# Kernel tuning notes

Measured on AMD Instinct MI355X. Metric: run time of the kernel, lower is better.

## Reference

```python
import jax, jax.numpy as jnp
import numpy as np

B, T, H, DK, DV = 4, 2048, 1024, 1024, 1024


def setup_inputs() -> dict:
    key = jax.random.key(0)
    ks = jax.random.split(key, 9)
    s = lambda fan_in: 1.0 / np.sqrt(fan_in)
    return {
        "y_all": jax.random.normal(ks[0], (B, T, H), dtype=jnp.float32),
        "Wq": jax.random.uniform(ks[1], (H, DK), jnp.float32, -s(H), s(H)),
        "bq": jax.random.uniform(ks[2], (DK,), jnp.float32, -s(H), s(H)),
        "Wk": jax.random.uniform(ks[3], (H, DK), jnp.float32, -s(H), s(H)),
        "bk": jax.random.uniform(ks[4], (DK,), jnp.float32, -s(H), s(H)),
        "Wv": jax.random.uniform(ks[5], (H, DV), jnp.float32, -s(H), s(H)),
        "bv": jax.random.uniform(ks[6], (DV,), jnp.float32, -s(H), s(H)),
        "Wo": jax.random.uniform(ks[7], (DV, H), jnp.float32, -s(DV), s(DV)),
        "bo": jax.random.uniform(ks[8], (H,), jnp.float32, -s(DV), s(DV)),
    }


def reference(y_all, Wq, bq, Wk, bk, Wv, bv, Wo, bo):
    # Fused causal attention equivalent to the per-timestep Python loop.
    dk = Wq.shape[1]
    q = (y_all @ Wq + bq) / jnp.sqrt(jnp.asarray(dk, y_all.dtype))  # [B,T,DK]
    k = y_all @ Wk + bk                                             # [B,T,DK]
    v = y_all @ Wv + bv                                             # [B,T,DV]
    scores = jnp.einsum("bqd,bkd->bqk", q, k)                       # [B,T,T]
    t = y_all.shape[1]
    causal = jnp.tril(jnp.ones((t, t), dtype=bool))                 # [T,T]
    scores = jnp.where(causal[None], scores, jnp.asarray(-jnp.inf, scores.dtype))
    w = jax.nn.softmax(scores, axis=-1)                             # [B,T,T]
    ctx = jnp.einsum("bqk,bkd->bqd", w, v)                          # [B,T,DV]
    return ctx @ Wo + bo                                            # [B,T,H]
```

## Files before the change

kernel.cpp:

```cpp
#include <hip/hip_runtime.h>
#include <hip/hip_bf16.h>
#include <cstdint>

#define DEVI __device__ __forceinline__

typedef __attribute__((ext_vector_type(8))) short bf16x8;
typedef __attribute__((ext_vector_type(4))) short bf16x4;
typedef __attribute__((ext_vector_type(4))) float f32x4;

DEVI short f2bf(float f) {
  unsigned u = __float_as_uint(f);
  u += 0x7fff + ((u >> 16) & 1);
  return (short)(u >> 16);
}
DEVI float bf2f(short s) { return __uint_as_float(((unsigned)(unsigned short)s) << 16); }

DEVI void gl_lds16(const short* g, short* l) {
  __builtin_amdgcn_global_load_lds((const __attribute__((address_space(1))) unsigned*)g,
                                   (__attribute__((address_space(3))) unsigned*)l, 16, 0, 0);
}

constexpr int BM = 128, BN = 128, BK = 64;

template<int MODE, int BIASMODE, bool OUTF32, int DECODE>
__global__ __launch_bounds__(256, 2)
void gemm_bt(const short* __restrict__ A, const short* __restrict__ B,
             void* __restrict__ Cv, const float* __restrict__ b0,
             float scale, int K, int lda, int ldb, int ldc,
             long long sA, long long sB, long long sC, int tdim)
{
  const int nwg = gridDim.x, orig = blockIdx.x;
  const int q8 = nwg >> 3, r8 = nwg & 7;
  const int xcd = orig & 7, idx8 = orig >> 3;
  const int wg = (xcd < r8 ? xcd * (q8 + 1) : r8 * (q8 + 1) + (xcd - r8) * q8) + idx8;
  const int bz = blockIdx.z;

  int bi = wg / tdim;
  const int bj = wg - bi * tdim;

  A += (long long)bz * sA;
  B += (long long)bz * sB;

  __shared__ __align__(16) short lA[2][BM * BK];
  __shared__ __align__(16) short lB[2][BN * BK];

  const int tid = threadIdx.x, wave = tid >> 6, lane = tid & 63;
  const int wr = wave >> 1, wc = wave & 1;
  const int brow = bi * BM, bcol = bj * BN;
  const int fr = lane & 15, h = lane >> 4;

  const int ck0 = ((h ^ (fr & 7))) * 8;
  const int swc = ((tid & 7) ^ ((tid >> 3) & 7)) * 8;
  const short* pA = A + (long long)(brow + (tid >> 3)) * lda + swc;
  const short* pB = B + (long long)(bcol + (tid >> 3)) * ldb + swc;

  f32x4 acc[4][4] = {};
  const int nt = K / BK;

  auto stage = [&](int buf, int t) {
    const long long ko = (long long)t * BK;
#pragma unroll
    for (int j = 0; j < 4; ++j)
      gl_lds16(pA + (long long)(j * 32) * lda + ko, &lA[buf][j * 2048 + tid * 8]);
#pragma unroll
    for (int j = 0; j < 4; ++j)
      gl_lds16(pB + (long long)(j * 32) * ldb + ko, &lB[buf][j * 2048 + tid * 8]);
  };

  stage(0, 0);
  __syncthreads();

  int cur = 0;
  for (int t = 0; t < nt; ++t) {
    if (t + 1 < nt) stage(cur ^ 1, t + 1);

    const short* bufA = lA[cur];
    const short* bufB = lB[cur];
    bf16x8 af[4], bg[4];
#pragma unroll
    for (int m = 0; m < 4; ++m)
      af[m] = *(const bf16x8*)&bufA[(wr * 64 + m * 16 + fr) * BK + ck0];
#pragma unroll
    for (int n = 0; n < 4; ++n)
      bg[n] = *(const bf16x8*)&bufB[(wc * 64 + n * 16 + fr) * BK + ck0];
#pragma unroll
    for (int m = 0; m < 4; ++m)
#pragma unroll
      for (int n = 0; n < 4; ++n)
        acc[m][n] = __builtin_amdgcn_mfma_f32_16x16x32_bf16(af[m], bg[n], acc[m][n], 0, 0, 0);
#pragma unroll
    for (int m = 0; m < 4; ++m)
      af[m] = *(const bf16x8*)&bufA[((wr * 64 + m * 16 + fr) * BK + ck0) ^ 32];
#pragma unroll
    for (int n = 0; n < 4; ++n)
      bg[n] = *(const bf16x8*)&bufB[((wc * 64 + n * 16 + fr) * BK + ck0) ^ 32];
#pragma unroll
    for (int m = 0; m < 4; ++m)
#pragma unroll
      for (int n = 0; n < 4; ++n)
        acc[m][n] = __builtin_amdgcn_mfma_f32_16x16x32_bf16(af[m], bg[n], acc[m][n], 0, 0, 0);

    __syncthreads();
    cur ^= 1;
  }

  const int lrow = h * 4;
  float* Cf = (float*)Cv + (long long)bz * sC;
  short* Cs = (short*)Cv + (long long)bz * sC;
  int colg[4]; float bvv[4];
#pragma unroll
  for (int n = 0; n < 4; ++n) {
    colg[n] = bcol + wc * 64 + n * 16 + fr;
    bvv[n] = (BIASMODE == 1) ? b0[colg[n]] : 0.f;
  }
#pragma unroll
  for (int m = 0; m < 4; ++m) {
    const int row = brow + wr * 64 + m * 16 + lrow;
#pragma unroll
    for (int j = 0; j < 4; ++j) {
#pragma unroll
      for (int n = 0; n < 4; ++n) {
        const float val = (acc[m][n][j] + bvv[n]) * scale;
        if constexpr (OUTF32) Cf[(long long)(row + j) * ldc + colg[n]] = val;
        else                  Cs[(long long)(row + j) * ldc + colg[n]] = f2bf(val);
      }
    }
  }
}

__global__ __launch_bounds__(256, 4)
void gemm_g(const short* __restrict__ ybf, const short* __restrict__ MTb,
            short* __restrict__ G, const float* __restrict__ wvec)
{
  const int orig = blockIdx.x;
  const int xcd = orig & 7, idx8 = orig >> 3;
  const int wg = xcd * 64 + idx8;
  const int bi = wg >> 3, bj = wg & 7;

  __shared__ __align__(16) short lA[BM * BK];
  __shared__ __align__(16) short lB[BN * BK];

  const int tid = threadIdx.x, wave = tid >> 6, lane = tid & 63;
  const int wr = wave >> 1, wc = wave & 1;
  const int brow = bi * BM, bcol = bj * BN;
  const int fr = lane & 15, h = lane >> 4;

  const int ck0 = ((h ^ (fr & 7))) * 8;
  const int swc = ((tid & 7) ^ ((tid >> 3) & 7)) * 8;
  const short* pA = ybf + (long long)(brow + (tid >> 3)) * 1024 + swc;
  const short* pB = MTb + (long long)(bcol + (tid >> 3)) * 1024 + swc;

  f32x4 acc[4][4] = {};

  for (int t = 0; t < 16; ++t) {
    const long long ko = (long long)t * BK;
#pragma unroll
    for (int j = 0; j < 4; ++j)
      gl_lds16(pA + (long long)(j * 32) * 1024 + ko, &lA[j * 2048 + tid * 8]);
#pragma unroll
    for (int j = 0; j < 4; ++j)
      gl_lds16(pB + (long long)(j * 32) * 1024 + ko, &lB[j * 2048 + tid * 8]);
    __syncthreads();

    bf16x8 af[4], bg[4];
#pragma unroll
    for (int m = 0; m < 4; ++m)
      af[m] = *(const bf16x8*)&lA[(wr * 64 + m * 16 + fr) * BK + ck0];
#pragma unroll
    for (int n = 0; n < 4; ++n)
      bg[n] = *(const bf16x8*)&lB[(wc * 64 + n * 16 + fr) * BK + ck0];
#pragma unroll
    for (int m = 0; m < 4; ++m)
#pragma unroll
      for (int n = 0; n < 4; ++n)
        acc[m][n] = __builtin_amdgcn_mfma_f32_16x16x32_bf16(af[m], bg[n], acc[m][n], 0, 0, 0);
#pragma unroll
    for (int m = 0; m < 4; ++m)
      af[m] = *(const bf16x8*)&lA[((wr * 64 + m * 16 + fr) * BK + ck0) ^ 32];
#pragma unroll
    for (int n = 0; n < 4; ++n)
      bg[n] = *(const bf16x8*)&lB[((wc * 64 + n * 16 + fr) * BK + ck0) ^ 32];
#pragma unroll
    for (int m = 0; m < 4; ++m)
#pragma unroll
      for (int n = 0; n < 4; ++n)
        acc[m][n] = __builtin_amdgcn_mfma_f32_16x16x32_bf16(af[m], bg[n], acc[m][n], 0, 0, 0);
    __syncthreads();
  }

  const int lrow = h * 4;
  int colg[4]; float bvv[4];
#pragma unroll
  for (int n = 0; n < 4; ++n) {
    colg[n] = bcol + wc * 64 + n * 16 + fr;
    bvv[n] = wvec[colg[n]];
  }
#pragma unroll
  for (int m = 0; m < 4; ++m) {
    const int row = brow + wr * 64 + m * 16 + lrow;
#pragma unroll
    for (int j = 0; j < 4; ++j)
#pragma unroll
      for (int n = 0; n < 4; ++n)
        G[(long long)(row + j) * 1024 + colg[n]] =
            f2bf((acc[m][n][j] + bvv[n]) * (1.f / 32.f));
  }
}

__global__ __launch_bounds__(256, 4)
void gemm_sz(const short* __restrict__ G, const short* __restrict__ ybf,
             const short* __restrict__ WvoT, short* __restrict__ scores,
             short* __restrict__ zT)
{
  const int orig = blockIdx.x;
  const int xcd = orig & 7, idx8 = orig >> 3;
  const int wg = xcd * 132 + idx8;

  const short *A, *B; short* C; int ldc, bi, bj;
  if (wg < 544) {
    const int z = wg / 136, t = wg - z * 136;
    int b = (int)((__fsqrt_rn(8.f * (float)t + 1.f) - 1.f) * 0.5f);
    if ((b + 1) * (b + 2) / 2 <= t) ++b;
    if (b * (b + 1) / 2 > t) --b;
    bi = b; bj = t - b * (b + 1) / 2;
    A = G + (long long)z * 2048 * 1024;
    B = ybf + (long long)z * 2048 * 1024;
    C = scores + (long long)z * 2048 * 2048;
    ldc = 2048;
  } else {
    const int lwg = wg - 544;
    bi = lwg >> 6; bj = lwg & 63;
    A = WvoT; B = ybf; C = zT; ldc = 8192;
  }

  __shared__ __align__(16) short lA[BM * BK];
  __shared__ __align__(16) short lB[BN * BK];

  const int tid = threadIdx.x, wave = tid >> 6, lane = tid & 63;
  const int wr = wave >> 1, wc = wave & 1;
  const int brow = bi * BM, bcol = bj * BN;
  const int fr = lane & 15, h = lane >> 4;

  const int ck0 = ((h ^ (fr & 7))) * 8;
  const int swc = ((tid & 7) ^ ((tid >> 3) & 7)) * 8;
  const short* pA = A + (long long)(brow + (tid >> 3)) * 1024 + swc;
  const short* pB = B + (long long)(bcol + (tid >> 3)) * 1024 + swc;

  f32x4 acc[4][4] = {};

  for (int t = 0; t < 16; ++t) {
    const long long ko = (long long)t * BK;
#pragma unroll
    for (int j = 0; j < 4; ++j)
      gl_lds16(pA + (long long)(j * 32) * 1024 + ko, &lA[j * 2048 + tid * 8]);
#pragma unroll
    for (int j = 0; j < 4; ++j)
      gl_lds16(pB + (long long)(j * 32) * 1024 + ko, &lB[j * 2048 + tid * 8]);
    __syncthreads();

    bf16x8 af[4], bg[4];
#pragma unroll
    for (int m = 0; m < 4; ++m)
      af[m] = *(const bf16x8*)&lA[(wr * 64 + m * 16 + fr) * BK + ck0];
#pragma unroll
    for (int n = 0; n < 4; ++n)
      bg[n] = *(const bf16x8*)&lB[(wc * 64 + n * 16 + fr) * BK + ck0];
#pragma unroll
    for (int m = 0; m < 4; ++m)
#pragma unroll
      for (int n = 0; n < 4; ++n)
        acc[m][n] = __builtin_amdgcn_mfma_f32_16x16x32_bf16(af[m], bg[n], acc[m][n], 0, 0, 0);
#pragma unroll
    for (int m = 0; m < 4; ++m)
      af[m] = *(const bf16x8*)&lA[((wr * 64 + m * 16 + fr) * BK + ck0) ^ 32];
#pragma unroll
    for (int n = 0; n < 4; ++n)
      bg[n] = *(const bf16x8*)&lB[((wc * 64 + n * 16 + fr) * BK + ck0) ^ 32];
#pragma unroll
    for (int m = 0; m < 4; ++m)
#pragma unroll
      for (int n = 0; n < 4; ++n)
        acc[m][n] = __builtin_amdgcn_mfma_f32_16x16x32_bf16(af[m], bg[n], acc[m][n], 0, 0, 0);
    __syncthreads();
  }

  const int lrow = h * 4;
  int colg[4];
#pragma unroll
  for (int n = 0; n < 4; ++n) colg[n] = bcol + wc * 64 + n * 16 + fr;
#pragma unroll
  for (int m = 0; m < 4; ++m) {
    const int row = brow + wr * 64 + m * 16 + lrow;
#pragma unroll
    for (int j = 0; j < 4; ++j)
#pragma unroll
      for (int n = 0; n < 4; ++n)
        C[(long long)(row + j) * ldc + colg[n]] = f2bf(acc[m][n][j]);
  }
}

__global__ __launch_bounds__(256, 6)
void gemm_pv(const short* __restrict__ scores, const short* __restrict__ zT,
             float* __restrict__ out, const float* __restrict__ bias)
{
  const int orig = blockIdx.x;
  const int xcd = orig & 7, idx8 = orig >> 3;
  const int z = xcd >> 1;
  const int bi = ((idx8 >> 4) << 1) | (xcd & 1);
  const int bj = idx8 & 15;

  const short* A = scores + (long long)z * 2048 * 2048;
  const int nt = bi + 1;

  __shared__ __align__(16) short lA[64 * 64];
  __shared__ __align__(16) short lB[64 * 64];

  const int tid = threadIdx.x, wave = tid >> 6, lane = tid & 63;
  const int wm = wave >> 1, wn = wave & 1;
  const int brow = bi * 64, bcol = bj * 64;
  const int fr = lane & 15, h = lane >> 4;

  const int ck0 = ((h ^ (fr & 7))) * 8;
  const int swc = ((tid & 7) ^ ((tid >> 3) & 7)) * 8;
  const short* pA = A + (long long)(brow + (tid >> 3)) * 2048 + swc;
  const short* pB = zT + (long long)(bcol + (tid >> 3)) * 8192 + z * 2048 + swc;

  f32x4 acc[2][2] = {};

  for (int t = 0; t < nt; ++t) {
    const long long ko = (long long)t * 64;
#pragma unroll
    for (int j = 0; j < 2; ++j)
      gl_lds16(pA + (long long)(j * 32) * 2048 + ko, &lA[j * 2048 + tid * 8]);
#pragma unroll
    for (int j = 0; j < 2; ++j)
      gl_lds16(pB + (long long)(j * 32) * 8192 + ko, &lB[j * 2048 + tid * 8]);
    __syncthreads();

    bf16x8 af[2], bg[2];
#pragma unroll
    for (int m = 0; m < 2; ++m)
      af[m] = *(const bf16x8*)&lA[(wm * 32 + m * 16 + fr) * 64 + ck0];
#pragma unroll
    for (int n = 0; n < 2; ++n)
      bg[n] = *(const bf16x8*)&lB[(wn * 32 + n * 16 + fr) * 64 + ck0];
#pragma unroll
    for (int m = 0; m < 2; ++m)
#pragma unroll
      for (int n = 0; n < 2; ++n)
        acc[m][n] = __builtin_amdgcn_mfma_f32_16x16x32_bf16(af[m], bg[n], acc[m][n], 0, 0, 0);
#pragma unroll
    for (int m = 0; m < 2; ++m)
      af[m] = *(const bf16x8*)&lA[((wm * 32 + m * 16 + fr) * 64 + ck0) ^ 32];
#pragma unroll
    for (int n = 0; n < 2; ++n)
      bg[n] = *(const bf16x8*)&lB[((wn * 32 + n * 16 + fr) * 64 + ck0) ^ 32];
#pragma unroll
    for (int m = 0; m < 2; ++m)
#pragma unroll
      for (int n = 0; n < 2; ++n)
        acc[m][n] = __builtin_amdgcn_mfma_f32_16x16x32_bf16(af[m], bg[n], acc[m][n], 0, 0, 0);
    __syncthreads();
  }

  const int lrow = h * 4;
  int colg[2]; float bvv[2];
#pragma unroll
  for (int n = 0; n < 2; ++n) {
    colg[n] = bcol + wn * 32 + n * 16 + fr;
    bvv[n] = bias[colg[n]];
  }
#pragma unroll
  for (int m = 0; m < 2; ++m) {
    const int row = brow + wm * 32 + m * 16 + lrow;
#pragma unroll
    for (int j = 0; j < 4; ++j)
#pragma unroll
      for (int n = 0; n < 2; ++n)
        out[(long long)(z * 2048 + row + j) * 1024 + colg[n]] = acc[m][n][j] + bvv[n];
  }
}

__global__ __launch_bounds__(256)
void softmax_causal_bf16_k(short* __restrict__ sc)
{
  const int T = 2048;
  const long long row = blockIdx.x;
  const int t = (int)(row & (T - 1));
  short* ps = sc + row * (long long)T;
  const int tid = threadIdx.x, wave = tid >> 6, lane = tid & 63;
  const int c0 = tid * 8;
  const int wlim = ((t >> 6) + 1) << 6;

  bf16x8 v = {};
  if (c0 <= t) v = *(const bf16x8*)&ps[c0];
  float x[8];
#pragma unroll
  for (int j = 0; j < 8; ++j) x[j] = bf2f(v[j]);

  float mx = -3.0e38f;
#pragma unroll
  for (int j = 0; j < 8; ++j) if (c0 + j <= t) mx = fmaxf(mx, x[j]);
#pragma unroll
  for (int o = 32; o; o >>= 1) mx = fmaxf(mx, __shfl_xor(mx, o, 64));
  __shared__ float red[8];
  if (lane == 0) red[wave] = mx;
  __syncthreads();
  const float M = fmaxf(fmaxf(red[0], red[1]), fmaxf(red[2], red[3]));

  float e[8], s = 0.f;
#pragma unroll
  for (int j = 0; j < 8; ++j) { e[j] = (c0 + j <= t) ? __expf(x[j] - M) : 0.f; s += e[j]; }
#pragma unroll
  for (int o = 32; o; o >>= 1) s += __shfl_xor(s, o, 64);
  if (lane == 0) red[4 + wave] = s;
  __syncthreads();
  const float inv = 1.f / (red[4] + red[5] + red[6] + red[7]);

  if (c0 < wlim) {
    bf16x8 ov;
#pragma unroll
    for (int j = 0; j < 8; ++j) ov[j] = f2bf(e[j] * inv);
    *(bf16x8*)&ps[c0] = ov;
  }
}

__global__ __launch_bounds__(256)
void cvt_y_k(const float* __restrict__ y, short* __restrict__ ybf)
{
  const long long i = (long long)blockIdx.x * 256 + threadIdx.x;
  const float4 v0 = ((const float4*)y)[i * 2];
  const float4 v1 = ((const float4*)y)[i * 2 + 1];
  bf16x8 o;
  o[0] = f2bf(v0.x); o[1] = f2bf(v0.y); o[2] = f2bf(v0.z); o[3] = f2bf(v0.w);
  o[4] = f2bf(v1.x); o[5] = f2bf(v1.y); o[6] = f2bf(v1.z); o[7] = f2bf(v1.w);
  ((bf16x8*)ybf)[i] = o;
}

__global__ __launch_bounds__(256)
void cvt_w_all_k(const float* __restrict__ w0, const float* __restrict__ w1,
                 const float* __restrict__ w2, const float* __restrict__ w3,
                 short* __restrict__ o0, short* __restrict__ o1,
                 short* __restrict__ o2, short* __restrict__ o3)
{
  const int tx = threadIdx.x & 31, ty = threadIdx.x >> 5;
  const int r0 = blockIdx.y * 32, c0 = blockIdx.x * 32;
  if (blockIdx.z != 2) {
    const float* in = (blockIdx.z == 0) ? w0 : (blockIdx.z == 1 ? w1 : w3);
    short* out      = (blockIdx.z == 0) ? o0 : (blockIdx.z == 1 ? o1 : o3);
#pragma unroll
    for (int i = 0; i < 4; ++i)
      out[(long long)(r0 + ty + 8 * i) * 1024 + c0 + tx] =
          f2bf(in[(long long)(r0 + ty + 8 * i) * 1024 + c0 + tx]);
    return;
  }
  __shared__ float tile[32][33];
#pragma unroll
  for (int i = 0; i < 4; ++i)
    tile[ty + 8 * i][tx] = w2[(long long)(r0 + ty + 8 * i) * 1024 + c0 + tx];
  __syncthreads();
#pragma unroll
  for (int i = 0; i < 4; ++i)
    o2[(long long)(c0 + ty + 8 * i) * 1024 + r0 + tx] = f2bf(tile[tx][ty + 8 * i]);
}

__global__ __launch_bounds__(256)
void bias_init_k(const float* __restrict__ bo, float* __restrict__ outb)
{
  const int j = blockIdx.x * 256 + threadIdx.x;
  outb[j] = bo[j];
}

__global__ __launch_bounds__(256)
void bias_fold_k(const float* __restrict__ bv, const float* __restrict__ Wo,
                 float* __restrict__ outb)
{
  const int r0 = blockIdx.x * 16;
  const int c4 = threadIdx.x;
  float4 acc = make_float4(0.f, 0.f, 0.f, 0.f);
  for (int r = 0; r < 16; ++r) {
    const float s = bv[r0 + r];
    const float4 w = ((const float4*)(Wo + (long long)(r0 + r) * 1024))[c4];
    acc.x += s * w.x; acc.y += s * w.y; acc.z += s * w.z; acc.w += s * w.w;
  }
  atomicAdd(&outb[c4 * 4 + 0], acc.x);
  atomicAdd(&outb[c4 * 4 + 1], acc.y);
  atomicAdd(&outb[c4 * 4 + 2], acc.z);
  atomicAdd(&outb[c4 * 4 + 3], acc.w);
}

__global__ __launch_bounds__(256)
void wkbq_gemv_k(const float* __restrict__ Wk, const float* __restrict__ bq,
                 float* __restrict__ w)
{
  const int row = blockIdx.x, tid = threadIdx.x;
  const float4 a = ((const float4*)(Wk + (long long)row * 1024))[tid];
  const float4 b = ((const float4*)bq)[tid];
  float s = a.x * b.x + a.y * b.y + a.z * b.z + a.w * b.w;
#pragma unroll
  for (int o = 32; o; o >>= 1) s += __shfl_xor(s, o, 64);
  __shared__ float red[4];
  if ((tid & 63) == 0) red[tid >> 6] = s;
  __syncthreads();
  if (tid == 0) w[row] = red[0] + red[1] + red[2] + red[3];
}

__global__ __launch_bounds__(256)
void combine4_k(const float* __restrict__ p, short* __restrict__ out)
{
  const long long i = (long long)blockIdx.x * 256 + threadIdx.x;
  const float4 a = ((const float4*)p)[i];
  const float4 b = ((const float4*)(p + 1048576))[i];
  const float4 c = ((const float4*)(p + 2097152))[i];
  const float4 d = ((const float4*)(p + 3145728))[i];
  bf16x4 o;
  o[0] = f2bf(a.x + b.x + c.x + d.x);
  o[1] = f2bf(a.y + b.y + c.y + d.y);
  o[2] = f2bf(a.z + b.z + c.z + d.z);
  o[3] = f2bf(a.w + b.w + c.w + d.w);
  ((bf16x4*)out)[i] = o;
}

extern "C" void kernel_launch(void* const* d_in, const int* in_sizes, int n_in,
                              void* d_out, int out_size, void* d_ws, size_t ws_size,
                              hipStream_t stream)
{
  (void)in_sizes; (void)n_in; (void)out_size; (void)ws_size;
  const float* y  = (const float*)d_in[0];
  const float* Wq = (const float*)d_in[1];
  const float* bq = (const float*)d_in[2];
  const float* Wk = (const float*)d_in[3];
  const float* bk = (const float*)d_in[4];
  const float* Wv = (const float*)d_in[5];
  const float* bv = (const float*)d_in[6];
  const float* Wo = (const float*)d_in[7];
  const float* bo = (const float*)d_in[8];
  float* out = (float*)d_out;
  (void)bk;

  const int T = 2048;
  const long long MT = 8192;
  const long long MM = 1048576;

  short* ws    = (short*)d_ws;
  short* ybf   = ws;
  short* WqBf  = ybf + MT * 1024;
  short* WkBf  = WqBf + MM;
  short* WoT   = WkBf + MM;
  short* WvBf  = WoT + MM;
  short* MTb   = WvBf + MM;
  short* WvoT  = MTb + MM;
  short* G     = WvoT + MM;
  short* zT    = G + MT * 1024;
  short* scores = zT + MT * 1024;
  float* bvWoBo = (float*)(scores + 4ll * T * T);
  float* wvec   = bvWoBo + 1024;
  float* part   = wvec + 1024;

  cvt_y_k<<<4096, 256, 0, stream>>>(y, ybf);
  cvt_w_all_k<<<dim3(32, 32, 4), 256, 0, stream>>>(
      Wq, Wk, Wo, Wv, WqBf, WkBf, WoT, WvBf);
  bias_init_k<<<4, 256, 0, stream>>>(bo, bvWoBo);
  bias_fold_k<<<64, 256, 0, stream>>>(bv, Wo, bvWoBo);
  wkbq_gemv_k<<<1024, 256, 0, stream>>>(Wk, bq, wvec);

  gemm_bt<0, 0, true, 0><<<dim3(64, 1, 4), 256, 0, stream>>>(
      WkBf, WqBf, part, nullptr, 1.f, 256, 1024, 1024, 1024,
      256, 256, 1048576, 8);
  combine4_k<<<1024, 256, 0, stream>>>(part, MTb);

  gemm_bt<0, 0, true, 0><<<dim3(64, 1, 4), 256, 0, stream>>>(
      WoT, WvBf, part, nullptr, 1.f, 256, 1024, 1024, 1024,
      256, 256, 1048576, 8);
  combine4_k<<<1024, 256, 0, stream>>>(part, WvoT);

  gemm_g<<<512, 256, 0, stream>>>(ybf, MTb, G, wvec);

  gemm_sz<<<1056, 256, 0, stream>>>(G, ybf, WvoT, scores, zT);

  softmax_causal_bf16_k<<<(int)MT, 256, 0, stream>>>(scores);

  gemm_pv<<<2048, 256, 0, stream>>>(scores, zT, out, bvWoBo);
}
```

Measured before the change: 175.3 us.

## Merge prep kernels and weight GEMMs, retile G and score GEMMs for more workgroups

Merges the five conversion and bias pre-pass kernels into one launch, and merges the two split-K weight-product GEMMs and their two combine passes into single launches. gemm_g and gemm_sz are replaced by new versions launched with twice as many workgroups, likely smaller tiles, and the bias add for bo is folded into the final PV epilogue. The goal is fewer kernel launches and better CU occupancy on the mid-sized GEMMs. The cost is more branching inside the merged kernels and possibly less data reuse per tile.

New measurement: 162.6 us. 1.08x faster.

```diff
diff --git a/kernel.cpp b/kernel.cpp
--- a/kernel.cpp
+++ b/kernel.cpp
@@ -20,225 +20,29 @@
                                    (__attribute__((address_space(3))) unsigned*)l, 16, 0, 0);
 }
 
-constexpr int BM = 128, BN = 128, BK = 64;
-
-template<int MODE, int BIASMODE, bool OUTF32, int DECODE>
-__global__ __launch_bounds__(256, 2)
-void gemm_bt(const short* __restrict__ A, const short* __restrict__ B,
-             void* __restrict__ Cv, const float* __restrict__ b0,
-             float scale, int K, int lda, int ldb, int ldc,
-             long long sA, long long sB, long long sC, int tdim)
-{
-  const int nwg = gridDim.x, orig = blockIdx.x;
-  const int q8 = nwg >> 3, r8 = nwg & 7;
-  const int xcd = orig & 7, idx8 = orig >> 3;
-  const int wg = (xcd < r8 ? xcd * (q8 + 1) : r8 * (q8 + 1) + (xcd - r8) * q8) + idx8;
-  const int bz = blockIdx.z;
-
-  int bi = wg / tdim;
-  const int bj = wg - bi * tdim;
-
-  A += (long long)bz * sA;
-  B += (long long)bz * sB;
-
-  __shared__ __align__(16) short lA[2][BM * BK];
-  __shared__ __align__(16) short lB[2][BN * BK];
-
-  const int tid = threadIdx.x, wave = tid >> 6, lane = tid & 63;
-  const int wr = wave >> 1, wc = wave & 1;
-  const int brow = bi * BM, bcol = bj * BN;
-  const int fr = lane & 15, h = lane >> 4;
-
-  const int ck0 = ((h ^ (fr & 7))) * 8;
-  const int swc = ((tid & 7) ^ ((tid >> 3) & 7)) * 8;
-  const short* pA = A + (long long)(brow + (tid >> 3)) * lda + swc;
-  const short* pB = B + (long long)(bcol + (tid >> 3)) * ldb + swc;
-
-  f32x4 acc[4][4] = {};
-  const int nt = K / BK;
-
-  auto stage = [&](int buf, int t) {
-    const long long ko = (long long)t * BK;
-#pragma unroll
-    for (int j = 0; j < 4; ++j)
-      gl_lds16(pA + (long long)(j * 32) * lda + ko, &lA[buf][j * 2048 + tid * 8]);
-#pragma unroll
-    for (int j = 0; j < 4; ++j)
-      gl_lds16(pB + (long long)(j * 32) * ldb + ko, &lB[buf][j * 2048 + tid * 8]);
-  };
-
-  stage(0, 0);
-  __syncthreads();
-
-  int cur = 0;
-  for (int t = 0; t < nt; ++t) {
-    if (t + 1 < nt) stage(cur ^ 1, t + 1);
-
-    const short* bufA = lA[cur];
-    const short* bufB = lB[cur];
-    bf16x8 af[4], bg[4];
-#pragma unroll
-    for (int m = 0; m < 4; ++m)
-      af[m] = *(const bf16x8*)&bufA[(wr * 64 + m * 16 + fr) * BK + ck0];
-#pragma unroll
-    for (int n = 0; n < 4; ++n)
-      bg[n] = *(const bf16x8*)&bufB[(wc * 64 + n * 16 + fr) * BK + ck0];
-#pragma unroll
-    for (int m = 0; m < 4; ++m)
-#pragma unroll
-      for (int n = 0; n < 4; ++n)
-        acc[m][n] = __builtin_amdgcn_mfma_f32_16x16x32_bf16(af[m], bg[n], acc[m][n], 0, 0, 0);
-#pragma unroll
-    for (int m = 0; m < 4; ++m)
-      af[m] = *(const bf16x8*)&bufA[((wr * 64 + m * 16 + fr) * BK + ck0) ^ 32];
-#pragma unroll
-    for (int n = 0; n < 4; ++n)
-      bg[n] = *(const bf16x8*)&bufB[((wc * 64 + n * 16 + fr) * BK + ck0) ^ 32];
-#pragma unroll
-    for (int m = 0; m < 4; ++m)
-#pragma unroll
-      for (int n = 0; n < 4; ++n)
-        acc[m][n] = __builtin_amdgcn_mfma_f32_16x16x32_bf16(af[m], bg[n], acc[m][n], 0, 0, 0);
-
-    __syncthreads();
-    cur ^= 1;
-  }
-
-  const int lrow = h * 4;
-  float* Cf = (float*)Cv + (long long)bz * sC;
-  short* Cs = (short*)Cv + (long long)bz * sC;
-  int colg[4]; float bvv[4];
-#pragma unroll
-  for (int n = 0; n < 4; ++n) {
-    colg[n] = bcol + wc * 64 + n * 16 + fr;
-    bvv[n] = (BIASMODE == 1) ? b0[colg[n]] : 0.f;
-  }
-#pragma unroll
-  for (int m = 0; m < 4; ++m) {
-    const int row = brow + wr * 64 + m * 16 + lrow;
-#pragma unroll
-    for (int j = 0; j < 4; ++j) {
-#pragma unroll
-      for (int n = 0; n < 4; ++n) {
-        const float val = (acc[m][n][j] + bvv[n]) * scale;
-        if constexpr (OUTF32) Cf[(long long)(row + j) * ldc + colg[n]] = val;
-        else                  Cs[(long long)(row + j) * ldc + colg[n]] = f2bf(val);
-      }
-    }
-  }
-}
 
 __global__ __launch_bounds__(256, 4)
-void gemm_g(const short* __restrict__ ybf, const short* __restrict__ MTb,
-            short* __restrict__ G, const float* __restrict__ wvec)
+void gemm_ww(const short* __restrict__ WkBf, const short* __restrict__ WqBf,
+             const short* __restrict__ WoT, const short* __restrict__ WvBf,
+             float* __restrict__ partM, float* __restrict__ partW)
 {
   const int orig = blockIdx.x;
   const int xcd = orig & 7, idx8 = orig >> 3;
   const int wg = xcd * 64 + idx8;
-  const int bi = wg >> 3, bj = wg & 7;
-
-  __shared__ __align__(16) short lA[BM * BK];
-  __shared__ __align__(16) short lB[BN * BK];
+  const int job = wg >> 8, rem = wg & 255;
+  const int z = rem >> 6, t = rem & 63;
+  const int bi = t >> 3, bj = t & 7;
+
+  const short* A = job ? WoT  : WkBf;
+  const short* B = job ? WvBf : WqBf;
+  float* Cf = (job ? partW : partM) + (long long)z * 1048576;
+
+  __shared__ __align__(16) short lA[128 * 64];
+  __shared__ __align__(16) short lB[128 * 64];
 
   const int tid = threadIdx.x, wave = tid >> 6, lane = tid & 63;
   const int wr = wave >> 1, wc = wave & 1;
-  const int brow = bi * BM, bcol = bj * BN;
-  const int fr = lane & 15, h = lane >> 4;
-
-  const int ck0 = ((h ^ (fr & 7))) * 8;
-  const int swc = ((tid & 7) ^ ((tid >> 3) & 7)) * 8;
-  const short* pA = ybf + (long long)(brow + (tid >> 3)) * 1024 + swc;
-  const short* pB = MTb + (long long)(bcol + (tid >> 3)) * 1024 + swc;
-
-  f32x4 acc[4][4] = {};
-
-  for (int t = 0; t < 16; ++t) {
-    const long long ko = (long long)t * BK;
-#pragma unroll
-    for (int j = 0; j < 4; ++j)
-      gl_lds16(pA + (long long)(j * 32) * 1024 + ko, &lA[j * 2048 + tid * 8]);
-#pragma unroll
-    for (int j = 0; j < 4; ++j)
-      gl_lds16(pB + (long long)(j * 32) * 1024 + ko, &lB[j * 2048 + tid * 8]);
-    __syncthreads();
-
-    bf16x8 af[4], bg[4];
-#pragma unroll
-    for (int m = 0; m < 4; ++m)
-      af[m] = *(const bf16x8*)&lA[(wr * 64 + m * 16 + fr) * BK + ck0];
-#pragma unroll
-    for (int n = 0; n < 4; ++n)
-      bg[n] = *(const bf16x8*)&lB[(wc * 64 + n * 16 + fr) * BK + ck0];
-#pragma unroll
-    for (int m = 0; m < 4; ++m)
-#pragma unroll
-      for (int n = 0; n < 4; ++n)
-        acc[m][n] = __builtin_amdgcn_mfma_f32_16x16x32_bf16(af[m], bg[n], acc[m][n], 0, 0, 0);
-#pragma unroll
-    for (int m = 0; m < 4; ++m)
-      af[m] = *(const bf16x8*)&lA[((wr * 64 + m * 16 + fr) * BK + ck0) ^ 32];
-#pragma unroll
-    for (int n = 0; n < 4; ++n)
-      bg[n] = *(const bf16x8*)&lB[((wc * 64 + n * 16 + fr) * BK + ck0) ^ 32];
-#pragma unroll
-    for (int m = 0; m < 4; ++m)
-#pragma unroll
-      for (int n = 0; n < 4; ++n)
-        acc[m][n] = __builtin_amdgcn_mfma_f32_16x16x32_bf16(af[m], bg[n], acc[m][n], 0, 0, 0);
-    __syncthreads();
-  }
-
-  const int lrow = h * 4;
-  int colg[4]; float bvv[4];
-#pragma unroll
-  for (int n = 0; n < 4; ++n) {
-    colg[n] = bcol + wc * 64 + n * 16 + fr;
-    bvv[n] = wvec[colg[n]];
-  }
-#pragma unroll
-  for (int m = 0; m < 4; ++m) {
-    const int row = brow + wr * 64 + m * 16 + lrow;
-#pragma unroll
-    for (int j = 0; j < 4; ++j)
-#pragma unroll
-      for (int n = 0; n < 4; ++n)
-        G[(long long)(row + j) * 1024 + colg[n]] =
-            f2bf((acc[m][n][j] + bvv[n]) * (1.f / 32.f));
-  }
-}
-
-__global__ __launch_bounds__(256, 4)
-void gemm_sz(const short* __restrict__ G, const short* __restrict__ ybf,
-             const short* __restrict__ WvoT, short* __restrict__ scores,
-             short* __restrict__ zT)
-{
-  const int orig = blockIdx.x;
-  const int xcd = orig & 7, idx8 = orig >> 3;
-  const int wg = xcd * 132 + idx8;
-
-  const short *A, *B; short* C; int ldc, bi, bj;
-  if (wg < 544) {
-    const int z = wg / 136, t = wg - z * 136;
-    int b = (int)((__fsqrt_rn(8.f * (float)t + 1.f) - 1.f) * 0.5f);
-    if ((b + 1) * (b + 2) / 2 <= t) ++b;
-    if (b * (b + 1) / 2 > t) --b;
-    bi = b; bj = t - b * (b + 1) / 2;
-    A = G + (long long)z * 2048 * 1024;
-    B = ybf + (long long)z * 2048 * 1024;
-    C = scores + (long long)z * 2048 * 2048;
-    ldc = 2048;
-  } else {
-    const int lwg = wg - 544;
-    bi = lwg >> 6; bj = lwg & 63;
-    A = WvoT; B = ybf; C = zT; ldc = 8192;
-  }
-
-  __shared__ __align__(16) short lA[BM * BK];
-  __shared__ __align__(16) short lB[BN * BK];
-
-  const int tid = threadIdx.x, wave = tid >> 6, lane = tid & 63;
-  const int wr = wave >> 1, wc = wave & 1;
-  const int brow = bi * BM, bcol = bj * BN;
+  const int brow = bi * 128, bcol = bj * 128;
   const int fr = lane & 15, h = lane >> 4;
 
   const int ck0 = ((h ^ (fr & 7))) * 8;
@@ -247,9 +51,10 @@
   const short* pB = B + (long long)(bcol + (tid >> 3)) * 1024 + swc;
 
   f32x4 acc[4][4] = {};
-
-  for (int t = 0; t < 16; ++t) {
-    const long long ko = (long long)t * BK;
+  const long long ko0 = (long long)z * 256;
+
+  for (int t2 = 0; t2 < 4; ++t2) {
+    const long long ko = ko0 + t2 * 64;
 #pragma unroll
     for (int j = 0; j < 4; ++j)
       gl_lds16(pA + (long long)(j * 32) * 1024 + ko, &lA[j * 2048 + tid * 8]);
@@ -261,10 +66,10 @@
     bf16x8 af[4], bg[4];
 #pragma unroll
     for (int m = 0; m < 4; ++m)
-      af[m] = *(const bf16x8*)&lA[(wr * 64 + m * 16 + fr) * BK + ck0];
+      af[m] = *(const bf16x8*)&lA[(wr * 64 + m * 16 + fr) * 64 + ck0];
 #pragma unroll
     for (int n = 0; n < 4; ++n)
-      bg[n] = *(const bf16x8*)&lB[(wc * 64 + n * 16 + fr) * BK + ck0];
+      bg[n] = *(const bf16x8*)&lB[(wc * 64 + n * 16 + fr) * 64 + ck0];
 #pragma unroll
     for (int m = 0; m < 4; ++m)
 #pragma unroll
@@ -272,10 +77,10 @@
         acc[m][n] = __builtin_amdgcn_mfma_f32_16x16x32_bf16(af[m], bg[n], acc[m][n], 0, 0, 0);
 #pragma unroll
     for (int m = 0; m < 4; ++m)
-      af[m] = *(const bf16x8*)&lA[((wr * 64 + m * 16 + fr) * BK + ck0) ^ 32];
+      af[m] = *(const bf16x8*)&lA[((wr * 64 + m * 16 + fr) * 64 + ck0) ^ 32];
 #pragma unroll
     for (int n = 0; n < 4; ++n)
-      bg[n] = *(const bf16x8*)&lB[((wc * 64 + n * 16 + fr) * BK + ck0) ^ 32];
+      bg[n] = *(const bf16x8*)&lB[((wc * 64 + n * 16 + fr) * 64 + ck0) ^ 32];
 #pragma unroll
     for (int m = 0; m < 4; ++m)
 #pragma unroll
@@ -285,9 +90,6 @@
   }
 
   const int lrow = h * 4;
-  int colg[4];
-#pragma unroll
-  for (int n = 0; n < 4; ++n) colg[n] = bcol + wc * 64 + n * 16 + fr;
 #pragma unroll
   for (int m = 0; m < 4; ++m) {
     const int row = brow + wr * 64 + m * 16 + lrow;
@@ -295,220 +97,18 @@
     for (int j = 0; j < 4; ++j)
 #pragma unroll
       for (int n = 0; n < 4; ++n)
-        C[(long long)(row + j) * ldc + colg[n]] = f2bf(acc[m][n][j]);
-  }
-}
-
-__global__ __launch_bounds__(256, 6)
-void gemm_pv(const short* __restrict__ scores, const short* __restrict__ zT,
-             float* __restrict__ out, const float* __restrict__ bias)
-{
-  const int orig = blockIdx.x;
-  const int xcd = orig & 7, idx8 = orig >> 3;
-  const int z = xcd >> 1;
-  const int bi = ((idx8 >> 4) << 1) | (xcd & 1);
-  const int bj = idx8 & 15;
-
-  const short* A = scores + (long long)z * 2048 * 2048;
-  const int nt = bi + 1;
-
-  __shared__ __align__(16) short lA[64 * 64];
-  __shared__ __align__(16) short lB[64 * 64];
-
-  const int tid = threadIdx.x, wave = tid >> 6, lane = tid & 63;
-  const int wm = wave >> 1, wn = wave & 1;
-  const int brow = bi * 64, bcol = bj * 64;
-  const int fr = lane & 15, h = lane >> 4;
-
-  const int ck0 = ((h ^ (fr & 7))) * 8;
-  const int swc = ((tid & 7) ^ ((tid >> 3) & 7)) * 8;
-  const short* pA = A + (long long)(brow + (tid >> 3)) * 2048 + swc;
-  const short* pB = zT + (long long)(bcol + (tid >> 3)) * 8192 + z * 2048 + swc;
-
-  f32x4 acc[2][2] = {};
-
-  for (int t = 0; t < nt; ++t) {
-    const long long ko = (long long)t * 64;
-#pragma unroll
-    for (int j = 0; j < 2; ++j)
-      gl_lds16(pA + (long long)(j * 32) * 2048 + ko, &lA[j * 2048 + tid * 8]);
-#pragma unroll
-    for (int j = 0; j < 2; ++j)
-      gl_lds16(pB + (long long)(j * 32) * 8192 + ko, &lB[j * 2048 + tid * 8]);
-    __syncthreads();
-
-    bf16x8 af[2], bg[2];
-#pragma unroll
-    for (int m = 0; m < 2; ++m)
-      af[m] = *(const bf16x8*)&lA[(wm * 32 + m * 16 + fr) * 64 + ck0];
-#pragma unroll
-    for (int n = 0; n < 2; ++n)
-      bg[n] = *(const bf16x8*)&lB[(wn * 32 + n * 16 + fr) * 64 + ck0];
-#pragma unroll
-    for (int m = 0; m < 2; ++m)
-#pragma unroll
-      for (int n = 0; n < 2; ++n)
-        acc[m][n] = __builtin_amdgcn_mfma_f32_16x16x32_bf16(af[m], bg[n], acc[m][n], 0, 0, 0);
-#pragma unroll
-    for (int m = 0; m < 2; ++m)
-      af[m] = *(const bf16x8*)&lA[((wm * 32 + m * 16 + fr) * 64 + ck0) ^ 32];
-#pragma unroll
-    for (int n = 0; n < 2; ++n)
-      bg[n] = *(const bf16x8*)&lB[((wn * 32 + n * 16 + fr) * 64 + ck0) ^ 32];
-#pragma unroll
-    for (int m = 0; m < 2; ++m)
-#pragma unroll
-      for (int n = 0; n < 2; ++n)
-        acc[m][n] = __builtin_amdgcn_mfma_f32_16x16x32_bf16(af[m], bg[n], acc[m][n], 0, 0, 0);
-    __syncthreads();
-  }
-
-  const int lrow = h * 4;
-  int colg[2]; float bvv[2];
-#pragma unroll
-  for (int n = 0; n < 2; ++n) {
-    colg[n] = bcol + wn * 32 + n * 16 + fr;
-    bvv[n] = bias[colg[n]];
-  }
-#pragma unroll
-  for (int m = 0; m < 2; ++m) {
-    const int row = brow + wm * 32 + m * 16 + lrow;
-#pragma unroll
-    for (int j = 0; j < 4; ++j)
-#pragma unroll
-      for (int n = 0; n < 2; ++n)
-        out[(long long)(z * 2048 + row + j) * 1024 + colg[n]] = acc[m][n][j] + bvv[n];
+        Cf[(long long)(row + j) * 1024 + bcol + wc * 64 + n * 16 + fr] = acc[m][n][j];
   }
 }
 
 __global__ __launch_bounds__(256)
-void softmax_causal_bf16_k(short* __restrict__ sc)
-{
-  const int T = 2048;
-  const long long row = blockIdx.x;
-  const int t = (int)(row & (T - 1));
-  short* ps = sc + row * (long long)T;
-  const int tid = threadIdx.x, wave = tid >> 6, lane = tid & 63;
-  const int c0 = tid * 8;
-  const int wlim = ((t >> 6) + 1) << 6;
-
-  bf16x8 v = {};
-  if (c0 <= t) v = *(const bf16x8*)&ps[c0];
-  float x[8];
-#pragma unroll
-  for (int j = 0; j < 8; ++j) x[j] = bf2f(v[j]);
-
-  float mx = -3.0e38f;
-#pragma unroll
-  for (int j = 0; j < 8; ++j) if (c0 + j <= t) mx = fmaxf(mx, x[j]);
-#pragma unroll
-  for (int o = 32; o; o >>= 1) mx = fmaxf(mx, __shfl_xor(mx, o, 64));
-  __shared__ float red[8];
-  if (lane == 0) red[wave] = mx;
-  __syncthreads();
-  const float M = fmaxf(fmaxf(red[0], red[1]), fmaxf(red[2], red[3]));
-
-  float e[8], s = 0.f;
-#pragma unroll
-  for (int j = 0; j < 8; ++j) { e[j] = (c0 + j <= t) ? __expf(x[j] - M) : 0.f; s += e[j]; }
-#pragma unroll
-  for (int o = 32; o; o >>= 1) s += __shfl_xor(s, o, 64);
-  if (lane == 0) red[4 + wave] = s;
-  __syncthreads();
-  const float inv = 1.f / (red[4] + red[5] + red[6] + red[7]);
-
-  if (c0 < wlim) {
-    bf16x8 ov;
-#pragma unroll
-    for (int j = 0; j < 8; ++j) ov[j] = f2bf(e[j] * inv);
-    *(bf16x8*)&ps[c0] = ov;
-  }
-}
-
-__global__ __launch_bounds__(256)
-void cvt_y_k(const float* __restrict__ y, short* __restrict__ ybf)
-{
-  const long long i = (long long)blockIdx.x * 256 + threadIdx.x;
-  const float4 v0 = ((const float4*)y)[i * 2];
-  const float4 v1 = ((const float4*)y)[i * 2 + 1];
-  bf16x8 o;
-  o[0] = f2bf(v0.x); o[1] = f2bf(v0.y); o[2] = f2bf(v0.z); o[3] = f2bf(v0.w);
-  o[4] = f2bf(v1.x); o[5] = f2bf(v1.y); o[6] = f2bf(v1.z); o[7] = f2bf(v1.w);
-  ((bf16x8*)ybf)[i] = o;
-}
-
-__global__ __launch_bounds__(256)
-void cvt_w_all_k(const float* __restrict__ w0, const float* __restrict__ w1,
-                 const float* __restrict__ w2, const float* __restrict__ w3,
-                 short* __restrict__ o0, short* __restrict__ o1,
-                 short* __restrict__ o2, short* __restrict__ o3)
-{
-  const int tx = threadIdx.x & 31, ty = threadIdx.x >> 5;
-  const int r0 = blockIdx.y * 32, c0 = blockIdx.x * 32;
-  if (blockIdx.z != 2) {
-    const float* in = (blockIdx.z == 0) ? w0 : (blockIdx.z == 1 ? w1 : w3);
-    short* out      = (blockIdx.z == 0) ? o0 : (blockIdx.z == 1 ? o1 : o3);
-#pragma unroll
-    for (int i = 0; i < 4; ++i)
-      out[(long long)(r0 + ty + 8 * i) * 1024 + c0 + tx] =
-          f2bf(in[(long long)(r0 + ty + 8 * i) * 1024 + c0 + tx]);
-    return;
-  }
-  __shared__ float tile[32][33];
-#pragma unroll
-  for (int i = 0; i < 4; ++i)
-    tile[ty + 8 * i][tx] = w2[(long long)(r0 + ty + 8 * i) * 1024 + c0 + tx];
-  __syncthreads();
-#pragma unroll
-  for (int i = 0; i < 4; ++i)
-    o2[(long long)(c0 + ty + 8 * i) * 1024 + r0 + tx] = f2bf(tile[tx][ty + 8 * i]);
-}
-
-__global__ __launch_bounds__(256)
-void bias_init_k(const float* __restrict__ bo, float* __restrict__ outb)
-{
-  const int j = blockIdx.x * 256 + threadIdx.x;
-  outb[j] = bo[j];
-}
-
-__global__ __launch_bounds__(256)
-void bias_fold_k(const float* __restrict__ bv, const float* __restrict__ Wo,
-                 float* __restrict__ outb)
-{
-  const int r0 = blockIdx.x * 16;
-  const int c4 = threadIdx.x;
-  float4 acc = make_float4(0.f, 0.f, 0.f, 0.f);
-  for (int r = 0; r < 16; ++r) {
-    const float s = bv[r0 + r];
-    const float4 w = ((const float4*)(Wo + (long long)(r0 + r) * 1024))[c4];
-    acc.x += s * w.x; acc.y += s * w.y; acc.z += s * w.z; acc.w += s * w.w;
-  }
-  atomicAdd(&outb[c4 * 4 + 0], acc.x);
-  atomicAdd(&outb[c4 * 4 + 1], acc.y);
-  atomicAdd(&outb[c4 * 4 + 2], acc.z);
-  atomicAdd(&outb[c4 * 4 + 3], acc.w);
-}
-
-__global__ __launch_bounds__(256)
-void wkbq_gemv_k(const float* __restrict__ Wk, const float* __restrict__ bq,
-                 float* __restrict__ w)
-{
-  const int row = blockIdx.x, tid = threadIdx.x;
-  const float4 a = ((const float4*)(Wk + (long long)row * 1024))[tid];
-  const float4 b = ((const float4*)bq)[tid];
-  float s = a.x * b.x + a.y * b.y + a.z * b.z + a.w * b.w;
-#pragma unroll
-  for (int o = 32; o; o >>= 1) s += __shfl_xor(s, o, 64);
-  __shared__ float red[4];
-  if ((tid & 63) == 0) red[tid >> 6] = s;
-  __syncthreads();
-  if (tid == 0) w[row] = red[0] + red[1] + red[2] + red[3];
-}
-
-__global__ __launch_bounds__(256)
-void combine4_k(const float* __restrict__ p, short* __restrict__ out)
-{
-  const long long i = (long long)blockIdx.x * 256 + threadIdx.x;
+void combine_ww(const float* __restrict__ partM, const float* __restrict__ partW,
+                short* __restrict__ MTb, short* __restrict__ WvoT)
+{
+  const int wg = blockIdx.x;
+  const float* p = (wg < 1024) ? partM : partW;
+  short* out = (wg < 1024) ? MTb : WvoT;
+  const long long i = (long long)(wg & 1023) * 256 + threadIdx.x;
   const float4 a = ((const float4*)p)[i];
   const float4 b = ((const float4*)(p + 1048576))[i];
   const float4 c = ((const float4*)(p + 2097152))[i];
@@ -519,6 +119,373 @@
   o[2] = f2bf(a.z + b.z + c.z + d.z);
   o[3] = f2bf(a.w + b.w + c.w + d.w);
   ((bf16x4*)out)[i] = o;
+}
+
+__global__ __launch_bounds__(256, 6)
+void gemm_g2(const short* __restrict__ ybf, const short* __restrict__ MTb,
+             short* __restrict__ G, const float* __restrict__ wvec)
+{
+  const int orig = blockIdx.x;
+  const int xcd = orig & 7, idx8 = orig >> 3;
+  const int wg = xcd * 128 + idx8;
+  const int bi = wg >> 4, bj = wg & 15;
+
+  __shared__ __align__(16) short lA[128 * 64];
+  __shared__ __align__(16) short lB[64 * 64];
+
+  const int tid = threadIdx.x, wave = tid >> 6, lane = tid & 63;
+  const int wr = wave >> 1, wc = wave & 1;
+  const int brow = bi * 128, bcol = bj * 64;
+  const int fr = lane & 15, h = lane >> 4;
+
+  const int ck0 = ((h ^ (fr & 7))) * 8;
+  const int swc = ((tid & 7) ^ ((tid >> 3) & 7)) * 8;
+  const short* pA = ybf + (long long)(brow + (tid >> 3)) * 1024 + swc;
+  const short* pB = MTb + (long long)(bcol + (tid >> 3)) * 1024 + swc;
+
+  f32x4 acc[4][2] = {};
+
+  for (int t = 0; t < 16; ++t) {
+    const long long ko = (long long)t * 64;
+#pragma unroll
+    for (int j = 0; j < 4; ++j)
+      gl_lds16(pA + (long long)(j * 32) * 1024 + ko, &lA[j * 2048 + tid * 8]);
+#pragma unroll
+    for (int j = 0; j < 2; ++j)
+      gl_lds16(pB + (long long)(j * 32) * 1024 + ko, &lB[j * 2048 + tid * 8]);
+    __syncthreads();
+
+    bf16x8 af[4], bg[2];
+#pragma unroll
+    for (int m = 0; m < 4; ++m)
+      af[m] = *(const bf16x8*)&lA[(wr * 64 + m * 16 + fr) * 64 + ck0];
+#pragma unroll
+    for (int n = 0; n < 2; ++n)
+      bg[n] = *(const bf16x8*)&lB[(wc * 32 + n * 16 + fr) * 64 + ck0];
+#pragma unroll
+    for (int m = 0; m < 4; ++m)
+#pragma unroll
+      for (int n = 0; n < 2; ++n)
+        acc[m][n] = __builtin_amdgcn_mfma_f32_16x16x32_bf16(af[m], bg[n], acc[m][n], 0, 0, 0);
+#pragma unroll
+    for (int m = 0; m < 4; ++m)
+      af[m] = *(const bf16x8*)&lA[((wr * 64 + m * 16 + fr) * 64 + ck0) ^ 32];
+#pragma unroll
+    for (int n = 0; n < 2; ++n)
+      bg[n] = *(const bf16x8*)&lB[((wc * 32 + n * 16 + fr) * 64 + ck0) ^ 32];
+#pragma unroll
+    for (int m = 0; m < 4; ++m)
+#pragma unroll
+      for (int n = 0; n < 2; ++n)
+        acc[m][n] = __builtin_amdgcn_mfma_f32_16x16x32_bf16(af[m], bg[n], acc[m][n], 0, 0, 0);
+    __syncthreads();
+  }
+
+  const int lrow = h * 4;
+  int colg[2]; float bvv[2];
+#pragma unroll
+  for (int n = 0; n < 2; ++n) {
+    colg[n] = bcol + wc * 32 + n * 16 + fr;
+    bvv[n] = wvec[colg[n]];
+  }
+#pragma unroll
+  for (int m = 0; m < 4; ++m) {
+    const int row = brow + wr * 64 + m * 16 + lrow;
+#pragma unroll
+    for (int j = 0; j < 4; ++j)
+#pragma unroll
+      for (int n = 0; n < 2; ++n)
+        G[(long long)(row + j) * 1024 + colg[n]] =
+            f2bf((acc[m][n][j] + bvv[n]) * (1.f / 32.f));
+  }
+}
+
+__global__ __launch_bounds__(256, 6)
+void gemm_sz2(const short* __restrict__ G, const short* __restrict__ ybf,
+              const short* __restrict__ WvoT, short* __restrict__ scores,
+              short* __restrict__ zT)
+{
+  const int orig = blockIdx.x;
+  const int xcd = orig & 7, idx8 = orig >> 3;
+  const int wg = xcd * 264 + idx8;
+
+  const short *A, *B; short* C; int ldc, bi, bj;
+  if (wg < 1088) {
+    const int z = wg / 272, t = wg - z * 272;
+    int b = (int)((__fsqrt_rn(4.f * (float)t + 1.f) - 1.f) * 0.5f);
+    if ((b + 1) * (b + 2) <= t) ++b;
+    if (b * (b + 1) > t) --b;
+    bi = b; bj = t - b * (b + 1);
+    A = G + (long long)z * 2048 * 1024;
+    B = ybf + (long long)z * 2048 * 1024;
+    C = scores + (long long)z * 2048 * 2048;
+    ldc = 2048;
+  } else {
+    const int lwg = wg - 1088;
+    bi = lwg >> 7; bj = lwg & 127;
+    A = WvoT; B = ybf; C = zT; ldc = 8192;
+  }
+
+  __shared__ __align__(16) short lA[128 * 64];
+  __shared__ __align__(16) short lB[64 * 64];
+
+  const int tid = threadIdx.x, wave = tid >> 6, lane = tid & 63;
+  const int wr = wave >> 1, wc = wave & 1;
+  const int brow = bi * 128, bcol = bj * 64;
+  const int fr = lane & 15, h = lane >> 4;
+
+  const int ck0 = ((h ^ (fr & 7))) * 8;
+  const int swc = ((tid & 7) ^ ((tid >> 3) & 7)) * 8;
+  const short* pA = A + (long long)(brow + (tid >> 3)) * 1024 + swc;
+  const short* pB = B + (long long)(bcol + (tid >> 3)) * 1024 + swc;
+
+  f32x4 acc[4][2] = {};
+
+  for (int t = 0; t < 16; ++t) {
+    const long long ko = (long long)t * 64;
+#pragma unroll
+    for (int j = 0; j < 4; ++j)
+      gl_lds16(pA + (long long)(j * 32) * 1024 + ko, &lA[j * 2048 + tid * 8]);
+#pragma unroll
+    for (int j = 0; j < 2; ++j)
+      gl_lds16(pB + (long long)(j * 32) * 1024 + ko, &lB[j * 2048 + tid * 8]);
+    __syncthreads();
+
+    bf16x8 af[4], bg[2];
+#pragma unroll
+    for (int m = 0; m < 4; ++m)
+      af[m] = *(const bf16x8*)&lA[(wr * 64 + m * 16 + fr) * 64 + ck0];
+#pragma unroll
+    for (int n = 0; n < 2; ++n)
+      bg[n] = *(const bf16x8*)&lB[(wc * 32 + n * 16 + fr) * 64 + ck0];
+#pragma unroll
+    for (int m = 0; m < 4; ++m)
+#pragma unroll
+      for (int n = 0; n < 2; ++n)
+        acc[m][n] = __builtin_amdgcn_mfma_f32_16x16x32_bf16(af[m], bg[n], acc[m][n], 0, 0, 0);
+#pragma unroll
+    for (int m = 0; m < 4; ++m)
+      af[m] = *(const bf16x8*)&lA[((wr * 64 + m * 16 + fr) * 64 + ck0) ^ 32];
+#pragma unroll
+    for (int n = 0; n < 2; ++n)
+      bg[n] = *(const bf16x8*)&lB[((wc * 32 + n * 16 + fr) * 64 + ck0) ^ 32];
+#pragma unroll
+    for (int m = 0; m < 4; ++m)
+#pragma unroll
+      for (int n = 0; n < 2; ++n)
+        acc[m][n] = __builtin_amdgcn_mfma_f32_16x16x32_bf16(af[m], bg[n], acc[m][n], 0, 0, 0);
+    __syncthreads();
+  }
+
+  const int lrow = h * 4;
+  int colg[2];
+#pragma unroll
+  for (int n = 0; n < 2; ++n) colg[n] = bcol + wc * 32 + n * 16 + fr;
+#pragma unroll
+  for (int m = 0; m < 4; ++m) {
+    const int row = brow + wr * 64 + m * 16 + lrow;
+#pragma unroll
+    for (int j = 0; j < 4; ++j)
+#pragma unroll
+      for (int n = 0; n < 2; ++n)
+        C[(long long)(row + j) * ldc + colg[n]] = f2bf(acc[m][n][j]);
+  }
+}
+
+__global__ __launch_bounds__(256, 6)
+void gemm_pv(const short* __restrict__ scores, const short* __restrict__ zT,
+             float* __restrict__ out, const float* __restrict__ bo,
+             const float* __restrict__ bvWo)
+{
+  const int orig = blockIdx.x;
+  const int xcd = orig & 7, idx8 = orig >> 3;
+  const int z = xcd >> 1;
+  const int bi = ((idx8 >> 4) << 1) | (xcd & 1);
+  const int bj = idx8 & 15;
+
+  const short* A = scores + (long long)z * 2048 * 2048;
+  const int nt = bi + 1;
+
+  __shared__ __align__(16) short lA[64 * 64];
+  __shared__ __align__(16) short lB[64 * 64];
+
+  const int tid = threadIdx.x, wave = tid >> 6, lane = tid & 63;
+  const int wm = wave >> 1, wn = wave & 1;
+  const int brow = bi * 64, bcol = bj * 64;
+  const int fr = lane & 15, h = lane >> 4;
+
+  const int ck0 = ((h ^ (fr & 7))) * 8;
+  const int swc = ((tid & 7) ^ ((tid >> 3) & 7)) * 8;
+  const short* pA = A + (long long)(brow + (tid >> 3)) * 2048 + swc;
+  const short* pB = zT + (long long)(bcol + (tid >> 3)) * 8192 + z * 2048 + swc;
+
+  f32x4 acc[2][2] = {};
+
+  for (int t = 0; t < nt; ++t) {
+    const long long ko = (long long)t * 64;
+#pragma unroll
+    for (int j = 0; j < 2; ++j)
+      gl_lds16(pA + (long long)(j * 32) * 2048 + ko, &lA[j * 2048 + tid * 8]);
+#pragma unroll
+    for (int j = 0; j < 2; ++j)
+      gl_lds16(pB + (long long)(j * 32) * 8192 + ko, &lB[j * 2048 + tid * 8]);
+    __syncthreads();
+
+    bf16x8 af[2], bg[2];
+#pragma unroll
+    for (int m = 0; m < 2; ++m)
+      af[m] = *(const bf16x8*)&lA[(wm * 32 + m * 16 + fr) * 64 + ck0];
+#pragma unroll
+    for (int n = 0; n < 2; ++n)
+      bg[n] = *(const bf16x8*)&lB[(wn * 32 + n * 16 + fr) * 64 + ck0];
+#pragma unroll
+    for (int m = 0; m < 2; ++m)
+#pragma unroll
+      for (int n = 0; n < 2; ++n)
+        acc[m][n] = __builtin_amdgcn_mfma_f32_16x16x32_bf16(af[m], bg[n], acc[m][n], 0, 0, 0);
+#pragma unroll
+    for (int m = 0; m < 2; ++m)
+      af[m] = *(const bf16x8*)&lA[((wm * 32 + m * 16 + fr) * 64 + ck0) ^ 32];
+#pragma unroll
+    for (int n = 0; n < 2; ++n)
+      bg[n] = *(const bf16x8*)&lB[((wn * 32 + n * 16 + fr) * 64 + ck0) ^ 32];
+#pragma unroll
+    for (int m = 0; m < 2; ++m)
+#pragma unroll
+      for (int n = 0; n < 2; ++n)
+        acc[m][n] = __builtin_amdgcn_mfma_f32_16x16x32_bf16(af[m], bg[n], acc[m][n], 0, 0, 0);
+    __syncthreads();
+  }
+
+  const int lrow = h * 4;
+  int colg[2]; float bvv[2];
+#pragma unroll
+  for (int n = 0; n < 2; ++n) {
+    colg[n] = bcol + wn * 32 + n * 16 + fr;
+    bvv[n] = bo[colg[n]] + bvWo[colg[n]];
+  }
+#pragma unroll
+  for (int m = 0; m < 2; ++m) {
+    const int row = brow + wm * 32 + m * 16 + lrow;
+#pragma unroll
+    for (int j = 0; j < 4; ++j)
+#pragma unroll
+      for (int n = 0; n < 2; ++n)
+        out[(long long)(z * 2048 + row + j) * 1024 + colg[n]] = acc[m][n][j] + bvv[n];
+  }
+}
+
+__global__ __launch_bounds__(256)
+void softmax_causal_bf16_k(short* __restrict__ sc)
+{
+  const int T = 2048;
+  const long long row = blockIdx.x;
+  const int t = (int)(row & (T - 1));
+  short* ps = sc + row * (long long)T;
+  const int tid = threadIdx.x, wave = tid >> 6, lane = tid & 63;
+  const int c0 = tid * 8;
+  const int wlim = ((t >> 6) + 1) << 6;
+
+  bf16x8 v = {};
+  if (c0 <= t) v = *(const bf16x8*)&ps[c0];
+  float x[8];
+#pragma unroll
+  for (int j = 0; j < 8; ++j) x[j] = bf2f(v[j]);
+
+  float mx = -3.0e38f;
+#pragma unroll
+  for (int j = 0; j < 8; ++j) if (c0 + j <= t) mx = fmaxf(mx, x[j]);
+#pragma unroll
+  for (int o = 32; o; o >>= 1) mx = fmaxf(mx, __shfl_xor(mx, o, 64));
+  __shared__ float red[8];
+  if (lane == 0) red[wave] = mx;
+  __syncthreads();
+  const float M = fmaxf(fmaxf(red[0], red[1]), fmaxf(red[2], red[3]));
+
+  float e[8], s = 0.f;
+#pragma unroll
+  for (int j = 0; j < 8; ++j) { e[j] = (c0 + j <= t) ? __expf(x[j] - M) : 0.f; s += e[j]; }
+#pragma unroll
+  for (int o = 32; o; o >>= 1) s += __shfl_xor(s, o, 64);
+  if (lane == 0) red[4 + wave] = s;
+  __syncthreads();
+  const float inv = 1.f / (red[4] + red[5] + red[6] + red[7]);
+
+  if (c0 < wlim) {
+    bf16x8 ov;
+#pragma unroll
+    for (int j = 0; j < 8; ++j) ov[j] = f2bf(e[j] * inv);
+    *(bf16x8*)&ps[c0] = ov;
+  }
+}
+
+__global__ __launch_bounds__(256)
+void cvt_all(const float* __restrict__ y, const float* __restrict__ Wq,
+             const float* __restrict__ Wk, const float* __restrict__ Wo,
+             const float* __restrict__ Wv, const float* __restrict__ bq,
+             const float* __restrict__ bv,
+             short* __restrict__ ybf, short* __restrict__ WqBf,
+             short* __restrict__ WkBf, short* __restrict__ WoT,
+             short* __restrict__ WvBf, float* __restrict__ wvec,
+             float* __restrict__ bvWo)
+{
+  const int wg = blockIdx.x, tid = threadIdx.x;
+  __shared__ float tile[32][33];
+  __shared__ float red[4];
+
+  if (wg < 4096) {
+    const long long i = (long long)wg * 256 + tid;
+    const float4 v0 = ((const float4*)y)[i * 2];
+    const float4 v1 = ((const float4*)y)[i * 2 + 1];
+    bf16x8 o;
+    o[0] = f2bf(v0.x); o[1] = f2bf(v0.y); o[2] = f2bf(v0.z); o[3] = f2bf(v0.w);
+    o[4] = f2bf(v1.x); o[5] = f2bf(v1.y); o[6] = f2bf(v1.z); o[7] = f2bf(v1.w);
+    ((bf16x8*)ybf)[i] = o;
+  } else if (wg < 8192) {
+    const int lwg = wg - 4096;
+    const int bx = lwg & 31, by = (lwg >> 5) & 31, bz = lwg >> 10;
+    const int tx = tid & 31, ty = tid >> 5;
+    const int r0 = by * 32, c0 = bx * 32;
+    if (bz != 2) {
+      const float* in = (bz == 0) ? Wq : (bz == 1 ? Wk : Wv);
+      short* out      = (bz == 0) ? WqBf : (bz == 1 ? WkBf : WvBf);
+#pragma unroll
+      for (int i = 0; i < 4; ++i)
+        out[(long long)(r0 + ty + 8 * i) * 1024 + c0 + tx] =
+            f2bf(in[(long long)(r0 + ty + 8 * i) * 1024 + c0 + tx]);
+    } else {
+#pragma unroll
+      for (int i = 0; i < 4; ++i)
+        tile[ty + 8 * i][tx] = Wo[(long long)(r0 + ty + 8 * i) * 1024 + c0 + tx];
+      __syncthreads();
+#pragma unroll
+      for (int i = 0; i < 4; ++i)
+        WoT[(long long)(c0 + ty + 8 * i) * 1024 + r0 + tx] = f2bf(tile[tx][ty + 8 * i]);
+    }
+  } else if (wg < 9216) {
+    const int row = wg - 8192;
+    const float4 a = ((const float4*)(Wk + (long long)row * 1024))[tid];
+    const float4 b = ((const float4*)bq)[tid];
+    float s = a.x * b.x + a.y * b.y + a.z * b.z + a.w * b.w;
+#pragma unroll
+    for (int o = 32; o; o >>= 1) s += __shfl_xor(s, o, 64);
+    if ((tid & 63) == 0) red[tid >> 6] = s;
+    __syncthreads();
+    if (tid == 0) wvec[row] = red[0] + red[1] + red[2] + red[3];
+  } else {
+    const int r0 = (wg - 9216) * 16;
+    const int c4 = tid;
+    float4 acc = make_float4(0.f, 0.f, 0.f, 0.f);
+    for (int r = 0; r < 16; ++r) {
+      const float s = bv[r0 + r];
+      const float4 w = ((const float4*)(Wo + (long long)(r0 + r) * 1024))[c4];
+      acc.x += s * w.x; acc.y += s * w.y; acc.z += s * w.z; acc.w += s * w.w;
+    }
+    atomicAdd(&bvWo[c4 * 4 + 0], acc.x);
+    atomicAdd(&bvWo[c4 * 4 + 1], acc.y);
+    atomicAdd(&bvWo[c4 * 4 + 2], acc.z);
+    atomicAdd(&bvWo[c4 * 4 + 3], acc.w);
+  }
 }
 
 extern "C" void kernel_launch(void* const* d_in, const int* in_sizes, int n_in,
@@ -553,32 +520,24 @@
   short* G     = WvoT + MM;
   short* zT    = G + MT * 1024;
   short* scores = zT + MT * 1024;
-  float* bvWoBo = (float*)(scores + 4ll * T * T);
-  float* wvec   = bvWoBo + 1024;
-  float* part   = wvec + 1024;
-
-  cvt_y_k<<<4096, 256, 0, stream>>>(y, ybf);
-  cvt_w_all_k<<<dim3(32, 32, 4), 256, 0, stream>>>(
-      Wq, Wk, Wo, Wv, WqBf, WkBf, WoT, WvBf);
-  bias_init_k<<<4, 256, 0, stream>>>(bo, bvWoBo);
-  bias_fold_k<<<64, 256, 0, stream>>>(bv, Wo, bvWoBo);
-  wkbq_gemv_k<<<1024, 256, 0, stream>>>(Wk, bq, wvec);
-
-  gemm_bt<0, 0, true, 0><<<dim3(64, 1, 4), 256, 0, stream>>>(
-      WkBf, WqBf, part, nullptr, 1.f, 256, 1024, 1024, 1024,
-      256, 256, 1048576, 8);
-  combine4_k<<<1024, 256, 0, stream>>>(part, MTb);
-
-  gemm_bt<0, 0, true, 0><<<dim3(64, 1, 4), 256, 0, stream>>>(
-      WoT, WvBf, part, nullptr, 1.f, 256, 1024, 1024, 1024,
-      256, 256, 1048576, 8);
-  combine4_k<<<1024, 256, 0, stream>>>(part, WvoT);
-
-  gemm_g<<<512, 256, 0, stream>>>(ybf, MTb, G, wvec);
-
-  gemm_sz<<<1056, 256, 0, stream>>>(G, ybf, WvoT, scores, zT);
+  float* bvWo  = (float*)(scores + 4ll * T * T);
+  float* wvec  = bvWo + 1024;
+  float* partM = wvec + 1024;
+  float* partW = partM + 4ll * MM;
+
+  hipMemsetAsync(bvWo, 0, 1024 * sizeof(float), stream);
+
+  cvt_all<<<9280, 256, 0, stream>>>(y, Wq, Wk, Wo, Wv, bq, bv,
+                                    ybf, WqBf, WkBf, WoT, WvBf, wvec, bvWo);
+
+  gemm_ww<<<512, 256, 0, stream>>>(WkBf, WqBf, WoT, WvBf, partM, partW);
+  combine_ww<<<2048, 256, 0, stream>>>(partM, partW, MTb, WvoT);
+
+  gemm_g2<<<1024, 256, 0, stream>>>(ybf, MTb, G, wvec);
+
+  gemm_sz2<<<2112, 256, 0, stream>>>(G, ybf, WvoT, scores, zT);
 
   softmax_causal_bf16_k<<<(int)MT, 256, 0, stream>>>(scores);
 
-  gemm_pv<<<2048, 256, 0, stream>>>(scores, zT, out, bvWoBo);
-}
+  gemm_pv<<<2048, 256, 0, stream>>>(scores, zT, out, bo, bvWo);
+}
```
